# Kernel tuning notes

Measured on AMD Instinct MI355X. Metric: run time of the kernel, lower is better.

Reference implementation:

```python
import jax, jax.numpy as jnp
import numpy as np

B, S, L, D, H, F, V = 8, 1024, 12, 768, 12, 3072, 21128
TITLE_LEN, CONTENTS_LEN = 64, 960
DH = D // H
NEG_INF = -1e9


def setup_inputs() -> dict:
    key = jax.random.key(0)
    ks = jax.random.split(key, 14)
    p = lambda k, shape: (0.02 * jax.random.normal(k, shape)).astype(jnp.float32)
    return {
        "x": jax.random.randint(ks[0], (B, S), 0, V),
        "y": jax.random.randint(ks[1], (B, CONTENTS_LEN), 0, V),
        "word_emb": p(ks[2], (V, D)),
        "pos_emb": p(ks[3], (S, D)),
        "type_emb": p(ks[4], (2, D)),
        "emb_ln_g": jnp.ones((D,), jnp.float32),
        "emb_ln_b": jnp.zeros((D,), jnp.float32),
        "Wq": p(ks[5], (L, D, D)), "bq": jnp.zeros((L, D), jnp.float32),
        "Wk": p(ks[6], (L, D, D)), "bk": jnp.zeros((L, D), jnp.float32),
        "Wv": p(ks[7], (L, D, D)), "bv": jnp.zeros((L, D), jnp.float32),
        "Wo": p(ks[8], (L, D, D)), "bo": jnp.zeros((L, D), jnp.float32),
        "ln1_g": jnp.ones((L, D), jnp.float32), "ln1_b": jnp.zeros((L, D), jnp.float32),
        "W1": p(ks[9], (L, D, F)), "b1": jnp.zeros((L, F), jnp.float32),
        "W2": p(ks[10], (L, F, D)), "b2": jnp.zeros((L, D), jnp.float32),
        "ln2_g": jnp.ones((L, D), jnp.float32), "ln2_b": jnp.zeros((L, D), jnp.float32),
        "cls_W": p(ks[11], (D, V)), "cls_b": jnp.zeros((V,), jnp.float32),
    }


def _ln(x, g, b):
    m = x.mean(-1, keepdims=True)
    v = jnp.mean((x - m) ** 2, -1, keepdims=True)
    return (x - m) * jax.lax.rsqrt(v + 1e-12) * g + b


def _forward(x, y, word_emb, pos_emb, type_emb, emb_ln_g, emb_ln_b,
             Wq, bq, Wk, bk, Wv, bv, Wo, bo, ln1_g, ln1_b,
             W1, b1, W2, b2, ln2_g, ln2_b, cls_W, cls_b):
    # prefix-LM mask: causal (tril) except fully-visible title block [S,S]
    mask = jnp.tril(jnp.ones((S, S), jnp.float32))
    mask = mask.at[:TITLE_LEN, :TITLE_LEN].set(1.0)
    bias = (1.0 - mask) * NEG_INF  # additive attention bias

    h = word_emb[x] + pos_emb[None, :, :] + type_emb[0]  # [B,S,D]
    h = _ln(h, emb_ln_g, emb_ln_b)

    scale = 1.0 / np.sqrt(DH).astype(np.float32)

    def step(h, p):
        Wq_, bq_, Wk_, bk_, Wv_, bv_, Wo_, bo_, g1, bb1, W1_, bf1, W2_, bf2, g2, bb2 = p
        q = (h @ Wq_ + bq_).reshape(B, S, H, DH)
        k = (h @ Wk_ + bk_).reshape(B, S, H, DH)
        v = (h @ Wv_ + bv_).reshape(B, S, H, DH)
        scores = jnp.einsum('bqhd,bkhd->bhqk', q, k) * scale + bias  # [B,H,S,S]
        a = jax.nn.softmax(scores, axis=-1)
        ctx = jnp.einsum('bhqk,bkhd->bqhd', a, v).reshape(B, S, D)
        h = _ln(h + ctx @ Wo_ + bo_, g1, bb1)
        ffn = jax.nn.gelu(h @ W1_ + bf1, approximate=False) @ W2_ + bf2
        h = _ln(h + ffn, g2, bb2)
        return h, None

    h, _ = jax.lax.scan(step, h, (Wq, bq, Wk, bk, Wv, bv, Wo, bo,
                                  ln1_g, ln1_b, W1, b1, W2, b2, ln2_g, ln2_b))

    logits = h[:, -CONTENTS_LEN:, :] @ cls_W + cls_b  # [B,C,V]
    logp = jax.nn.log_softmax(logits, axis=-1)
    valid = (y != -100)
    yc = jnp.where(valid, y, 0)
    nll = -jnp.take_along_axis(logp, yc[..., None], axis=-1)[..., 0]
    return jnp.sum(nll * valid) / jnp.maximum(jnp.sum(valid), 1)


def reference(x, y, word_emb, pos_emb, type_emb, emb_ln_g, emb_ln_b,
              Wq, bq, Wk, bk, Wv, bv, Wo, bo, ln1_g, ln1_b,
              W1, b1, W2, b2, ln2_g, ln2_b, cls_W, cls_b):
    return _forward(x, y, word_emb, pos_emb, type_emb, emb_ln_g, emb_ln_b,
                    Wq, bq, Wk, bk, Wv, bv, Wo, bo, ln1_g, ln1_b,
                    W1, b1, W2, b2, ln2_g, ln2_b, cls_W, cls_b)
```

## Files before the change

kernel.cpp:

```cpp
#include <hip/hip_runtime.h>

#define BB 8
#define SS 1024
#define LL 12
#define DD 768
#define HH 12
#define FF 3072
#define VV 21128
#define DH 64
#define CLEN 960
#define NROWS (BB * CLEN)
#define TOKS (BB * SS)
#define NQKV 2304
#define QKW 1536

typedef __attribute__((ext_vector_type(8))) short bh8;
typedef __attribute__((ext_vector_type(4))) float f32x4;
typedef __attribute__((ext_vector_type(4))) unsigned short us4;

__device__ __forceinline__ float bf2f(unsigned short u) {
    union { unsigned int i; float f; } c; c.i = ((unsigned int)u) << 16; return c.f;
}
__device__ __forceinline__ unsigned short f2bf(float f) {
    union { float f; unsigned int i; } c; c.f = f;
    unsigned int r = c.i + 0x7fffu + ((c.i >> 16) & 1u);
    return (unsigned short)(r >> 16);
}

#define GLOAD16(gsrc, ldst)                                                              \
    __builtin_amdgcn_global_load_lds((const __attribute__((address_space(1))) unsigned int*)(gsrc), \
                                     (__attribute__((address_space(3))) unsigned int*)(ldst), 16, 0, 0)

__device__ __forceinline__ float bsum256(float v, float* red) {
#pragma unroll
    for (int o = 32; o; o >>= 1) v += __shfl_down(v, o);
    if ((threadIdx.x & 63) == 0) red[threadIdx.x >> 6] = v;
    __syncthreads();
    float r = red[0] + red[1] + red[2] + red[3];
    __syncthreads();
    return r;
}

__global__ void transpose_f32_bf16(const float* __restrict__ in, unsigned short* __restrict__ out,
                                   int R, int C) {
    __shared__ float tile[32][33];
    int c0 = blockIdx.x << 5, r0 = blockIdx.y << 5;
    int tx = threadIdx.x, ty = threadIdx.y;
    for (int i = ty; i < 32; i += 8) {
        int r = r0 + i, c = c0 + tx;
        if (r < R && c < C) tile[i][tx] = in[(size_t)r * C + c];
    }
    __syncthreads();
    for (int i = ty; i < 32; i += 8) {
        int oc = c0 + i, orr = r0 + tx;
        if (oc < C && orr < R) out[(size_t)oc * R + orr] = f2bf(tile[tx][i]);
    }
}

__global__ void transpose_layer(const float* __restrict__ Wq, const float* __restrict__ Wk,
                                const float* __restrict__ Wv, const float* __restrict__ Wo,
                                const float* __restrict__ W1, const float* __restrict__ W2,
                                unsigned short* __restrict__ wqkvT, unsigned short* __restrict__ woT,
                                unsigned short* __restrict__ w1T, unsigned short* __restrict__ w2T) {
    __shared__ float tile[32][33];
    int t = blockIdx.x;
    const float* src;
    unsigned short* dst;
    int R, C, txt, tt;
    if (t < 1728) {
        int which = t / 576; tt = t % 576;
        src = which == 0 ? Wq : (which == 1 ? Wk : Wv);
        dst = wqkvT + (size_t)which * DD * DD; R = DD; C = DD; txt = 24;
    } else if (t < 2304) {
        tt = t - 1728; src = Wo; dst = woT; R = DD; C = DD; txt = 24;
    } else if (t < 4608) {
        tt = t - 2304; src = W1; dst = w1T; R = DD; C = FF; txt = 96;
    } else {
        tt = t - 4608; src = W2; dst = w2T; R = FF; C = DD; txt = 24;
    }
    int c0 = (tt % txt) << 5, r0 = (tt / txt) << 5;
    int tx = threadIdx.x, ty = threadIdx.y;
    for (int i = ty; i < 32; i += 8) tile[i][tx] = src[(size_t)(r0 + i) * C + c0 + tx];
    __syncthreads();
    for (int i = ty; i < 32; i += 8) dst[(size_t)(c0 + i) * R + r0 + tx] = f2bf(tile[tx][i]);
}

__global__ void concat_bias_all(const float* __restrict__ bq, const float* __restrict__ bk,
                                const float* __restrict__ bv, float* __restrict__ out) {
    int i = blockIdx.x * 256 + threadIdx.x;
    if (i >= LL * NQKV) return;
    int l = i / NQKV, c = i % NQKV;
    float v = c < DD ? bq[(size_t)l * DD + c]
                     : (c < 2 * DD ? bk[(size_t)l * DD + c - DD] : bv[(size_t)l * DD + c - 2 * DD]);
    out[i] = v;
}

__global__ __launch_bounds__(256) void embed_ln(const int* __restrict__ x, const float* __restrict__ we,
                                                const float* __restrict__ pe, const float* __restrict__ te,
                                                const float* __restrict__ g, const float* __restrict__ be,
                                                unsigned short* __restrict__ hb) {
    int row = blockIdx.x;
    int s = row & (SS - 1);
    int tok = x[row];
    int tid = threadIdx.x;
    __shared__ float red[4];
    float v[3];
#pragma unroll
    for (int i = 0; i < 3; i++) {
        int c = tid + i * 256;
        v[i] = we[(size_t)tok * DD + c] + pe[(size_t)s * DD + c] + te[c];
    }
    float mean = bsum256(v[0] + v[1] + v[2], red) * (1.f / DD);
    float d0 = v[0] - mean, d1 = v[1] - mean, d2 = v[2] - mean;
    float var = bsum256(d0 * d0 + d1 * d1 + d2 * d2, red) * (1.f / DD);
    float inv = rsqrtf(var + 1e-12f);
    size_t base = (size_t)row * DD;
#pragma unroll
    for (int i = 0; i < 3; i++) {
        int c = tid + i * 256;
        hb[base + c] = f2bf((v[i] - mean) * inv * g[c] + be[c]);
    }
}

__global__ __launch_bounds__(256) void add_ln(const unsigned short* __restrict__ res,
                                              const unsigned short* __restrict__ t,
                                              const float* __restrict__ g, const float* __restrict__ be,
                                              unsigned short* __restrict__ outb) {
    int row = blockIdx.x;
    int tid = threadIdx.x;
    __shared__ float red[4];
    size_t base = (size_t)row * DD;
    float v[3];
#pragma unroll
    for (int i = 0; i < 3; i++) {
        int c = tid + i * 256;
        v[i] = bf2f(res[base + c]) + bf2f(t[base + c]);
    }
    float mean = bsum256(v[0] + v[1] + v[2], red) * (1.f / DD);
    float d0 = v[0] - mean, d1 = v[1] - mean, d2 = v[2] - mean;
    float var = bsum256(d0 * d0 + d1 * d1 + d2 * d2, red) * (1.f / DD);
    float inv = rsqrtf(var + 1e-12f);
#pragma unroll
    for (int i = 0; i < 3; i++) {
        int c = tid + i * 256;
        outb[base + c] = f2bf((v[i] - mean) * inv * g[c] + be[c]);
    }
}

template <int MODE>
__global__ __launch_bounds__(256) void gemm128(const unsigned short* __restrict__ A,
                                               const unsigned short* __restrict__ BT,
                                               const float* __restrict__ bias, void* __restrict__ Cp,
                                               int M, int N, int K, int ldc, int SM,
                                               unsigned short* __restrict__ vt_out,
                                               const int* __restrict__ yv,
                                               float* __restrict__ stS, float* __restrict__ stT) {
    __shared__ __align__(16) unsigned short As[2][128 * 32];
    __shared__ __align__(16) unsigned short Bs[2][128 * 32];
    const int tid = threadIdx.x;
    const int lane = tid & 63, w = tid >> 6;
    const int fr = lane & 15, fg = lane >> 4;
    const int wr = w >> 1, wc = w & 1;

    const int Nt = gridDim.x;
    const int flat = blockIdx.y * Nt + blockIdx.x;
    const int per8 = (Nt * gridDim.y) >> 3;
    const int virt = (flat & 7) * per8 + (flat >> 3);
    const int bandSz = SM * Nt;
    const int band = virt / bandSz, rem = virt - band * bandSz;
    const int nt = rem / SM;
    const int mt = band * SM + (rem - nt * SM);
    const int m0 = mt << 7, n0 = nt << 7;

    const int srow = lane >> 2;
    const int skcol = (lane & 3) << 3;

    int arow0 = m0 + (w * 2 + 0) * 16 + srow;
    int arow1 = m0 + (w * 2 + 1) * 16 + srow;
    int brow0 = n0 + (w * 2 + 0) * 16 + srow;
    int brow1 = n0 + (w * 2 + 1) * 16 + srow;
    if (brow0 >= N) brow0 = N - 1;
    if (brow1 >= N) brow1 = N - 1;
    const unsigned short* aptr0 = A + (size_t)arow0 * K + skcol;
    const unsigned short* aptr1 = A + (size_t)arow1 * K + skcol;
    const unsigned short* bptr0 = BT + (size_t)brow0 * K + skcol;
    const unsigned short* bptr1 = BT + (size_t)brow1 * K + skcol;

    auto stage = [&](int bf, int k0) {
        GLOAD16(aptr0 + k0, &As[bf][(w * 2 + 0) * 512]);
        GLOAD16(aptr1 + k0, &As[bf][(w * 2 + 1) * 512]);
        GLOAD16(bptr0 + k0, &Bs[bf][(w * 2 + 0) * 512]);
        GLOAD16(bptr1 + k0, &Bs[bf][(w * 2 + 1) * 512]);
    };

    f32x4 acc[4][4] = {};
    stage(0, 0);
    __syncthreads();
    int cur = 0;
    for (int k0 = 0; k0 < K; k0 += 32) {
        if (k0 + 32 < K) stage(cur ^ 1, k0 + 32);
        bh8 a[4], b[4];
#pragma unroll
        for (int mi = 0; mi < 4; mi++) a[mi] = *(const bh8*)&As[cur][(wr * 64 + mi * 16 + fr) * 32 + fg * 8];
#pragma unroll
        for (int ni = 0; ni < 4; ni++) b[ni] = *(const bh8*)&Bs[cur][(wc * 64 + ni * 16 + fr) * 32 + fg * 8];
        __builtin_amdgcn_s_setprio(1);
#pragma unroll
        for (int mi = 0; mi < 4; mi++)
#pragma unroll
            for (int ni = 0; ni < 4; ni++)
                acc[mi][ni] = __builtin_amdgcn_mfma_f32_16x16x32_bf16(a[mi], b[ni], acc[mi][ni], 0, 0, 0);
        __builtin_amdgcn_s_setprio(0);
        __syncthreads();
        cur ^= 1;
    }

    unsigned short* Cb = (unsigned short*)Cp;
#pragma unroll
    for (int mi = 0; mi < 4; mi++) {
        int rbase = m0 + wr * 64 + mi * 16 + fg * 4;
        if (MODE == 3) {
            float e[4] = {0.f, 0.f, 0.f, 0.f};
            int yr[4];
#pragma unroll
            for (int r = 0; r < 4; r++) yr[r] = yv[rbase + r];
#pragma unroll
            for (int ni = 0; ni < 4; ni++) {
                int col = n0 + wc * 64 + ni * 16 + fr;
                if (col < N) {
                    float bb = bias[col];
#pragma unroll
                    for (int r = 0; r < 4; r++) {
                        float v = acc[mi][ni][r] + bb;
                        e[r] += __expf(v);
                        if (col == yr[r]) stT[rbase + r] = v;
                    }
                }
            }
#pragma unroll
            for (int r = 0; r < 4; r++) {
#pragma unroll
                for (int off = 1; off < 16; off <<= 1) e[r] += __shfl_xor(e[r], off);
                if (fr == 0) atomicAdd(&stS[rbase + r], e[r]);
            }
        } else {
#pragma unroll
            for (int ni = 0; ni < 4; ni++) {
                int col = n0 + wc * 64 + ni * 16 + fr;
                if (MODE == 4) {
                    float bb = bias[col];
                    if (col < 2 * DD) {
#pragma unroll
                        for (int r = 0; r < 4; r++)
                            Cb[(size_t)(rbase + r) * QKW + col] = f2bf(acc[mi][ni][r] + bb);
                    } else {
                        int g = col - 2 * DD, h = g >> 6, d = g & 63;
                        int bi = rbase >> 10, s0 = rbase & 1023;
                        us4 val;
#pragma unroll
                        for (int r = 0; r < 4; r++) val[r] = f2bf(acc[mi][ni][r] + bb);
                        *(us4*)&vt_out[(((size_t)bi * HH + h) * DH + d) * SS + s0] = val;
                    }
                } else if (col < N) {
                    float bb = bias[col];
#pragma unroll
                    for (int r = 0; r < 4; r++) {
                        float v = acc[mi][ni][r] + bb;
                        if (MODE == 2) v = 0.5f * v * (1.0f + erff(v * 0.70710678118f));
                        Cb[(size_t)(rbase + r) * ldc + col] = f2bf(v);
                    }
                }
            }
        }
    }
}

__global__ __launch_bounds__(256) void flash_attn(const unsigned short* __restrict__ qkbuf,
                                                  const unsigned short* __restrict__ VT,
                                                  unsigned short* __restrict__ ctxb) {
    const int bx = blockIdx.x;
    const int h = blockIdx.y, b = blockIdx.z;
    const int tid = threadIdx.x;
    const int lane = tid & 63, w = tid >> 6;
    const int fr = lane & 15, fg = lane >> 4;
    __shared__ unsigned short Qs[64][68];
    __shared__ unsigned short Ks[64][68];
    __shared__ unsigned short Vt[64][68];
    __shared__ unsigned short Ps[4][16][68];

    const int srow = tid >> 2, sd0 = (tid & 3) << 4;
    const unsigned short* kbase = qkbuf + (size_t)(b * SS + srow) * QKW + DD + h * 64 + sd0;
    const unsigned short* vbase = VT + (((size_t)b * HH + h) * DH + srow) * SS + sd0;

    bh8 kr0, kr1, vr0, vr1;
    auto ld_reg = [&](int kt) {
        const unsigned short* ks = kbase + (size_t)(kt * 64) * QKW;
        kr0 = *(const bh8*)ks;
        kr1 = *(const bh8*)(ks + 8);
        const unsigned short* vs = vbase + kt * 64;
        vr0 = *(const bh8*)vs;
        vr1 = *(const bh8*)(vs + 8);
    };

    for (int half = 0; half < 2; half++) {
        const int qt = (half == 0) ? 15 - bx : bx;
        __syncthreads();
        {
            const unsigned short* src = qkbuf + (size_t)(b * SS + qt * 64 + srow) * QKW + h * 64 + sd0;
            *(bh8*)&Qs[srow][sd0] = *(const bh8*)src;
            *(bh8*)&Qs[srow][sd0 + 8] = *(const bh8*)(src + 8);
        }

        f32x4 o[4] = {};
        float m[4], l[4];
#pragma unroll
        for (int r = 0; r < 4; r++) { m[r] = -3e30f; l[r] = 0.f; }

        const int nkt = (qt == 0) ? 1 : qt + 1;
        ld_reg(0);
        for (int kt = 0; kt < nkt; kt++) {
            __syncthreads();
            *(bh8*)&Ks[srow][sd0] = kr0;
            *(bh8*)&Ks[srow][sd0 + 8] = kr1;
            *(bh8*)&Vt[srow][sd0] = vr0;
            *(bh8*)&Vt[srow][sd0 + 8] = vr1;
            if (kt + 1 < nkt) ld_reg(kt + 1);
            __syncthreads();

            f32x4 s[4] = {};
            bh8 a0 = *(const bh8*)&Qs[w * 16 + fr][fg * 8];
            bh8 a1 = *(const bh8*)&Qs[w * 16 + fr][32 + fg * 8];
            __builtin_amdgcn_s_setprio(1);
#pragma unroll
            for (int cf = 0; cf < 4; cf++) {
                bh8 b0 = *(const bh8*)&Ks[cf * 16 + fr][fg * 8];
                bh8 b1 = *(const bh8*)&Ks[cf * 16 + fr][32 + fg * 8];
                s[cf] = __builtin_amdgcn_mfma_f32_16x16x32_bf16(a0, b0, s[cf], 0, 0, 0);
                s[cf] = __builtin_amdgcn_mfma_f32_16x16x32_bf16(a1, b1, s[cf], 0, 0, 0);
            }
            __builtin_amdgcn_s_setprio(0);

            const bool diag = (qt > 0) && (kt == qt);
#pragma unroll
            for (int cf = 0; cf < 4; cf++) {
#pragma unroll
                for (int r = 0; r < 4; r++) {
                    float v = s[cf][r] * 0.125f;
                    if (diag) {
                        int key = cf * 16 + fr;
                        int qrow = w * 16 + fg * 4 + r;
                        if (key > qrow) v = -1e30f;
                    }
                    s[cf][r] = v;
                }
            }
            float sc[4], mn[4];
#pragma unroll
            for (int r = 0; r < 4; r++) {
                float v = fmaxf(fmaxf(s[0][r], s[1][r]), fmaxf(s[2][r], s[3][r]));
#pragma unroll
                for (int off = 1; off < 16; off <<= 1) v = fmaxf(v, __shfl_xor(v, off));
                mn[r] = fmaxf(m[r], v);
                sc[r] = __expf(m[r] - mn[r]);
                m[r] = mn[r];
            }
#pragma unroll
            for (int cf = 0; cf < 4; cf++) {
#pragma unroll
                for (int r = 0; r < 4; r++) s[cf][r] = __expf(s[cf][r] - mn[r]);
            }
#pragma unroll
            for (int r = 0; r < 4; r++) {
                float v = s[0][r] + s[1][r] + s[2][r] + s[3][r];
#pragma unroll
                for (int off = 1; off < 16; off <<= 1) v += __shfl_xor(v, off);
                l[r] = l[r] * sc[r] + v;
            }
#pragma unroll
            for (int df = 0; df < 4; df++) {
#pragma unroll
                for (int r = 0; r < 4; r++) o[df][r] *= sc[r];
            }
#pragma unroll
            for (int cf = 0; cf < 4; cf++) {
#pragma unroll
                for (int r = 0; r < 4; r++) Ps[w][fg * 4 + r][cf * 16 + fr] = f2bf(s[cf][r]);
            }
            bh8 pa0 = *(const bh8*)&Ps[w][fr][fg * 8];
            bh8 pa1 = *(const bh8*)&Ps[w][fr][32 + fg * 8];
            __builtin_amdgcn_s_setprio(1);
#pragma unroll
            for (int df = 0; df < 4; df++) {
                bh8 vb0 = *(const bh8*)&Vt[df * 16 + fr][fg * 8];
                bh8 vb1 = *(const bh8*)&Vt[df * 16 + fr][32 + fg * 8];
                o[df] = __builtin_amdgcn_mfma_f32_16x16x32_bf16(pa0, vb0, o[df], 0, 0, 0);
                o[df] = __builtin_amdgcn_mfma_f32_16x16x32_bf16(pa1, vb1, o[df], 0, 0, 0);
            }
            __builtin_amdgcn_s_setprio(0);
        }
#pragma unroll
        for (int df = 0; df < 4; df++) {
#pragma unroll
            for (int r = 0; r < 4; r++) {
                int q = qt * 64 + w * 16 + fg * 4 + r;
                float v = o[df][r] / l[r];
                ctxb[(((size_t)b * SS + q) * HH + h) * DH + df * 16 + fr] = f2bf(v);
            }
        }
    }
}

__global__ void gather_rows(const unsigned short* __restrict__ hb, unsigned short* __restrict__ hc,
                            float* __restrict__ stS, float* __restrict__ stT) {
    int idx = blockIdx.x * 256 + threadIdx.x;
    if (idx < NROWS) { stS[idx] = 0.f; stT[idx] = 0.f; }
    if (idx >= NROWS * (DD / 8)) return;
    int g = idx / (DD / 8), c8 = (idx % (DD / 8)) * 8;
    int b = g / CLEN, cc = g % CLEN;
    *(bh8*)&hc[(size_t)g * DD + c8] = *(const bh8*)&hb[((size_t)(b * SS + 64 + cc)) * DD + c8];
}

__global__ __launch_bounds__(256) void final_reduce(const float* __restrict__ stS,
                                                    const float* __restrict__ stT, const int* __restrict__ y,
                                                    float* __restrict__ out) {
    int tid = threadIdx.x;
    float s = 0.f, c = 0.f;
    for (int i = tid; i < NROWS; i += 256) {
        if (y[i] != -100) {
            s += logf(stS[i]) - stT[i];
            c += 1.f;
        }
    }
    __shared__ float red[4];
    float gs = bsum256(s, red);
    float gc = bsum256(c, red);
    if (tid == 0) out[0] = gs / fmaxf(gc, 1.f);
}

extern "C" void kernel_launch(void* const* d_in, const int* in_sizes, int n_in,
                              void* d_out, int out_size, void* d_ws, size_t ws_size,
                              hipStream_t stream) {
    const int* x = (const int*)d_in[0];
    const int* y = (const int*)d_in[1];
    const float* we = (const float*)d_in[2];
    const float* pe = (const float*)d_in[3];
    const float* te = (const float*)d_in[4];
    const float* eg = (const float*)d_in[5];
    const float* eb = (const float*)d_in[6];
    const float* Wq = (const float*)d_in[7];
    const float* bq = (const float*)d_in[8];
    const float* Wk = (const float*)d_in[9];
    const float* bk = (const float*)d_in[10];
    const float* Wv = (const float*)d_in[11];
    const float* bv = (const float*)d_in[12];
    const float* Wo = (const float*)d_in[13];
    const float* bo = (const float*)d_in[14];
    const float* g1 = (const float*)d_in[15];
    const float* b1n = (const float*)d_in[16];
    const float* W1 = (const float*)d_in[17];
    const float* b1 = (const float*)d_in[18];
    const float* W2 = (const float*)d_in[19];
    const float* b2 = (const float*)d_in[20];
    const float* g2 = (const float*)d_in[21];
    const float* b2n = (const float*)d_in[22];
    const float* clsW = (const float*)d_in[23];
    const float* clsb = (const float*)d_in[24];
    float* out = (float*)d_out;

    char* ws = (char*)d_ws;
    size_t off = 0;
    auto alloc = [&](size_t n) {
        void* p = ws + off;
        off += n;
        off = (off + 255) & ~(size_t)255;
        return p;
    };
    unsigned short* hb   = (unsigned short*)alloc((size_t)TOKS * DD * 2);
    unsigned short* h1b  = (unsigned short*)alloc((size_t)TOKS * DD * 2);
    unsigned short* tmpb = (unsigned short*)alloc((size_t)TOKS * DD * 2);
    unsigned short* qkbuf = (unsigned short*)alloc((size_t)TOKS * QKW * 2);
    unsigned short* vtb  = (unsigned short*)alloc((size_t)TOKS * DD * 2);
    unsigned short* ctxb = (unsigned short*)alloc((size_t)TOKS * DD * 2);
    unsigned short* ffnb = (unsigned short*)alloc((size_t)TOKS * FF * 2);
    unsigned short* wqkvT = (unsigned short*)alloc((size_t)NQKV * DD * 2);
    unsigned short* woT = (unsigned short*)alloc((size_t)DD * DD * 2);
    unsigned short* w1T = (unsigned short*)alloc((size_t)DD * FF * 2);
    unsigned short* w2T = (unsigned short*)alloc((size_t)DD * FF * 2);
    unsigned short* clsT = (unsigned short*)alloc((size_t)VV * DD * 2);
    unsigned short* hc = (unsigned short*)alloc((size_t)NROWS * DD * 2);
    float* bqkv = (float*)alloc((size_t)LL * NQKV * 4);
    float* stS = (float*)alloc(NROWS * 4);
    float* stT = (float*)alloc(NROWS * 4);

    dim3 tb(32, 8);
    transpose_f32_bf16<<<dim3((VV + 31) / 32, DD / 32), tb, 0, stream>>>(clsW, clsT, DD, VV);
    concat_bias_all<<<(LL * NQKV + 255) / 256, 256, 0, stream>>>(bq, bk, bv, bqkv);
    embed_ln<<<TOKS, 256, 0, stream>>>(x, we, pe, te, eg, eb, hb);

    for (int l = 0; l < LL; l++) {
        transpose_layer<<<6912, tb, 0, stream>>>(Wq + (size_t)l * DD * DD, Wk + (size_t)l * DD * DD,
                                                 Wv + (size_t)l * DD * DD, Wo + (size_t)l * DD * DD,
                                                 W1 + (size_t)l * DD * FF, W2 + (size_t)l * FF * DD,
                                                 wqkvT, woT, w1T, w2T);

        gemm128<4><<<dim3(NQKV / 128, TOKS / 128), 256, 0, stream>>>(
            hb, wqkvT, bqkv + (size_t)l * NQKV,
            qkbuf, TOKS, NQKV, DD, NQKV, 8, vtb, nullptr, nullptr, nullptr);

        flash_attn<<<dim3(8, HH, BB), 256, 0, stream>>>(qkbuf, vtb, ctxb);

        gemm128<1><<<dim3(DD / 128, TOKS / 128), 256, 0, stream>>>(
            ctxb, woT, bo + (size_t)l * DD, tmpb,
            TOKS, DD, DD, DD, 8, nullptr, nullptr, nullptr, nullptr);
        add_ln<<<TOKS, 256, 0, stream>>>(hb, tmpb, g1 + (size_t)l * DD, b1n + (size_t)l * DD, h1b);

        gemm128<2><<<dim3(FF / 128, TOKS / 128), 256, 0, stream>>>(
            h1b, w1T, b1 + (size_t)l * FF, ffnb,
            TOKS, FF, DD, FF, 8, nullptr, nullptr, nullptr, nullptr);
        gemm128<1><<<dim3(DD / 128, TOKS / 128), 256, 0, stream>>>(
            ffnb, w2T, b2 + (size_t)l * DD, tmpb,
            TOKS, DD, FF, DD, 8, nullptr, nullptr, nullptr, nullptr);
        add_ln<<<TOKS, 256, 0, stream>>>(h1b, tmpb, g2 + (size_t)l * DD, b2n + (size_t)l * DD, hb);
    }

    gather_rows<<<(NROWS * (DD / 8) + 255) / 256, 256, 0, stream>>>(hb, hc, stS, stT);
    gemm128<3><<<dim3((VV + 127) / 128, NROWS / 128), 256, 0, stream>>>(hc, clsT, clsb, nullptr,
                                                                        NROWS, VV, DD, VV, 6, nullptr,
                                                                        y, stS, stT);
    final_reduce<<<1, 256, 0, stream>>>(stS, stT, y, out);
}
```

Before: 3.861 ms.

## Use 128-key tiles in flash attention and keep Q fragments in registers

The flash attention kernel now processes 128 keys per iteration instead of 64, which halves the number of loop iterations and the block-wide barriers. Q fragments are loaded straight from global memory into registers, so the Q shared-memory tile and its barrier go away. The causal mask is applied only on the last tile and uses a prefix-aware limit. Larger tiles raise register and LDS use, and on the diagonal tile some work is wasted on masked keys.

```diff
diff --git a/kernel.cpp b/kernel.cpp
--- a/kernel.cpp
+++ b/kernel.cpp
@@ -283,56 +283,53 @@
     const int tid = threadIdx.x;
     const int lane = tid & 63, w = tid >> 6;
     const int fr = lane & 15, fg = lane >> 4;
-    __shared__ unsigned short Qs[64][68];
-    __shared__ unsigned short Ks[64][68];
-    __shared__ unsigned short Vt[64][68];
-    __shared__ unsigned short Ps[4][16][68];
-
-    const int srow = tid >> 2, sd0 = (tid & 3) << 4;
-    const unsigned short* kbase = qkbuf + (size_t)(b * SS + srow) * QKW + DD + h * 64 + sd0;
-    const unsigned short* vbase = VT + (((size_t)b * HH + h) * DH + srow) * SS + sd0;
-
-    bh8 kr0, kr1, vr0, vr1;
+    __shared__ unsigned short Ks[128][68];
+    __shared__ unsigned short Vt[64][132];
+    __shared__ unsigned short Ps[4][16][132];
+
+    const int krow = tid >> 1, kcol = (tid & 1) << 5;
+    const int vrow = tid >> 2, vcol = (tid & 3) << 5;
+    const unsigned short* kbase = qkbuf + (size_t)(b * SS + krow) * QKW + DD + h * 64 + kcol;
+    const unsigned short* vbase = VT + ((size_t)(b * HH + h) * DH + vrow) * SS + vcol;
+
+    bh8 kr[4], vr[4];
     auto ld_reg = [&](int kt) {
-        const unsigned short* ks = kbase + (size_t)(kt * 64) * QKW;
-        kr0 = *(const bh8*)ks;
-        kr1 = *(const bh8*)(ks + 8);
-        const unsigned short* vs = vbase + kt * 64;
-        vr0 = *(const bh8*)vs;
-        vr1 = *(const bh8*)(vs + 8);
+        const unsigned short* ks = kbase + (size_t)(kt * 128) * QKW;
+#pragma unroll
+        for (int j = 0; j < 4; j++) kr[j] = *(const bh8*)(ks + j * 8);
+        const unsigned short* vs = vbase + kt * 128;
+#pragma unroll
+        for (int j = 0; j < 4; j++) vr[j] = *(const bh8*)(vs + j * 8);
     };
 
     for (int half = 0; half < 2; half++) {
         const int qt = (half == 0) ? 15 - bx : bx;
-        __syncthreads();
-        {
-            const unsigned short* src = qkbuf + (size_t)(b * SS + qt * 64 + srow) * QKW + h * 64 + sd0;
-            *(bh8*)&Qs[srow][sd0] = *(const bh8*)src;
-            *(bh8*)&Qs[srow][sd0 + 8] = *(const bh8*)(src + 8);
-        }
+        const int nkt = (qt + 2) >> 1;
+        const int qrow_g = qt * 64 + w * 16 + fr;
+
+        const unsigned short* qr = qkbuf + (size_t)(b * SS + qrow_g) * QKW + h * 64 + fg * 8;
+        const bh8 a0 = *(const bh8*)qr;
+        const bh8 a1 = *(const bh8*)(qr + 32);
 
         f32x4 o[4] = {};
         float m[4], l[4];
 #pragma unroll
         for (int r = 0; r < 4; r++) { m[r] = -3e30f; l[r] = 0.f; }
 
-        const int nkt = (qt == 0) ? 1 : qt + 1;
         ld_reg(0);
         for (int kt = 0; kt < nkt; kt++) {
             __syncthreads();
-            *(bh8*)&Ks[srow][sd0] = kr0;
-            *(bh8*)&Ks[srow][sd0 + 8] = kr1;
-            *(bh8*)&Vt[srow][sd0] = vr0;
-            *(bh8*)&Vt[srow][sd0 + 8] = vr1;
+#pragma unroll
+            for (int j = 0; j < 4; j++) *(bh8*)&Ks[krow][kcol + j * 8] = kr[j];
+#pragma unroll
+            for (int j = 0; j < 4; j++) *(bh8*)&Vt[vrow][vcol + j * 8] = vr[j];
             if (kt + 1 < nkt) ld_reg(kt + 1);
             __syncthreads();
 
-            f32x4 s[4] = {};
-            bh8 a0 = *(const bh8*)&Qs[w * 16 + fr][fg * 8];
-            bh8 a1 = *(const bh8*)&Qs[w * 16 + fr][32 + fg * 8];
+            f32x4 s[8] = {};
             __builtin_amdgcn_s_setprio(1);
 #pragma unroll
-            for (int cf = 0; cf < 4; cf++) {
+            for (int cf = 0; cf < 8; cf++) {
                 bh8 b0 = *(const bh8*)&Ks[cf * 16 + fr][fg * 8];
                 bh8 b1 = *(const bh8*)&Ks[cf * 16 + fr][32 + fg * 8];
                 s[cf] = __builtin_amdgcn_mfma_f32_16x16x32_bf16(a0, b0, s[cf], 0, 0, 0);
@@ -340,16 +337,17 @@
             }
             __builtin_amdgcn_s_setprio(0);
 
-            const bool diag = (qt > 0) && (kt == qt);
-#pragma unroll
-            for (int cf = 0; cf < 4; cf++) {
+            const bool lastT = (kt == nkt - 1);
+#pragma unroll
+            for (int cf = 0; cf < 8; cf++) {
 #pragma unroll
                 for (int r = 0; r < 4; r++) {
                     float v = s[cf][r] * 0.125f;
-                    if (diag) {
-                        int key = cf * 16 + fr;
-                        int qrow = w * 16 + fg * 4 + r;
-                        if (key > qrow) v = -1e30f;
+                    if (lastT) {
+                        int key = kt * 128 + cf * 16 + fr;
+                        int q = qt * 64 + w * 16 + fg * 4 + r;
+                        int lim = q < 64 ? 63 : q;
+                        if (key > lim) v = -1e30f;
                     }
                     s[cf][r] = v;
                 }
@@ -357,7 +355,9 @@
             float sc[4], mn[4];
 #pragma unroll
             for (int r = 0; r < 4; r++) {
-                float v = fmaxf(fmaxf(s[0][r], s[1][r]), fmaxf(s[2][r], s[3][r]));
+                float v = s[0][r];
+#pragma unroll
+                for (int cf = 1; cf < 8; cf++) v = fmaxf(v, s[cf][r]);
 #pragma unroll
                 for (int off = 1; off < 16; off <<= 1) v = fmaxf(v, __shfl_xor(v, off));
                 mn[r] = fmaxf(m[r], v);
@@ -365,13 +365,15 @@
                 m[r] = mn[r];
             }
 #pragma unroll
-            for (int cf = 0; cf < 4; cf++) {
+            for (int cf = 0; cf < 8; cf++) {
 #pragma unroll
                 for (int r = 0; r < 4; r++) s[cf][r] = __expf(s[cf][r] - mn[r]);
             }
 #pragma unroll
             for (int r = 0; r < 4; r++) {
-                float v = s[0][r] + s[1][r] + s[2][r] + s[3][r];
+                float v = s[0][r];
+#pragma unroll
+                for (int cf = 1; cf < 8; cf++) v += s[cf][r];
 #pragma unroll
                 for (int off = 1; off < 16; off <<= 1) v += __shfl_xor(v, off);
                 l[r] = l[r] * sc[r] + v;
@@ -382,19 +384,21 @@
                 for (int r = 0; r < 4; r++) o[df][r] *= sc[r];
             }
 #pragma unroll
-            for (int cf = 0; cf < 4; cf++) {
+            for (int cf = 0; cf < 8; cf++) {
 #pragma unroll
                 for (int r = 0; r < 4; r++) Ps[w][fg * 4 + r][cf * 16 + fr] = f2bf(s[cf][r]);
             }
-            bh8 pa0 = *(const bh8*)&Ps[w][fr][fg * 8];
-            bh8 pa1 = *(const bh8*)&Ps[w][fr][32 + fg * 8];
+            bh8 pa[4];
+#pragma unroll
+            for (int kk = 0; kk < 4; kk++) pa[kk] = *(const bh8*)&Ps[w][fr][kk * 32 + fg * 8];
             __builtin_amdgcn_s_setprio(1);
 #pragma unroll
             for (int df = 0; df < 4; df++) {
-                bh8 vb0 = *(const bh8*)&Vt[df * 16 + fr][fg * 8];
-                bh8 vb1 = *(const bh8*)&Vt[df * 16 + fr][32 + fg * 8];
-                o[df] = __builtin_amdgcn_mfma_f32_16x16x32_bf16(pa0, vb0, o[df], 0, 0, 0);
-                o[df] = __builtin_amdgcn_mfma_f32_16x16x32_bf16(pa1, vb1, o[df], 0, 0, 0);
+#pragma unroll
+                for (int kk = 0; kk < 4; kk++) {
+                    bh8 vb = *(const bh8*)&Vt[df * 16 + fr][kk * 32 + fg * 8];
+                    o[df] = __builtin_amdgcn_mfma_f32_16x16x32_bf16(pa[kk], vb, o[df], 0, 0, 0);
+                }
             }
             __builtin_amdgcn_s_setprio(0);
         }
```

After: 3.977 ms. +3.0%, slower.
